# Performance work log

Hardware: AMD Instinct MI355X
Metric: run time of the kernel (lower is better)

Reference implementation:

```python
import jax, jax.numpy as jnp
import numpy as np

D_MODEL = 1024
D_STATE = 16
LN_EPS = 1e-5


def setup_inputs() -> dict:
    key = jax.random.key(0)
    ks = jax.random.split(key, 10)
    B, L, D, N = 4, 1024, D_MODEL, D_STATE
    s = lambda fan_in: 1.0 / np.sqrt(fan_in)
    x_in = jax.random.normal(ks[0], (B, L, D), dtype=jnp.float32)
    W_in = jax.random.uniform(ks[1], (D, 2 * D), jnp.float32, -s(D), s(D))
    W_x = jax.random.uniform(ks[2], (D, D + 2 * N), jnp.float32, -s(D), s(D))
    W_dt = jax.random.uniform(ks[3], (D, D), jnp.float32, -s(D), s(D))
    b_dt = jax.random.uniform(ks[4], (D,), jnp.float32, -4.0, -1.0)
    A_log = jnp.tile(jnp.log(jnp.arange(1, N + 1, dtype=jnp.float32))[None, :], (D, 1))
    D_param = jnp.ones((D,), dtype=jnp.float32)
    W_out = jax.random.uniform(ks[5], (D, D), jnp.float32, -s(D), s(D))
    ln_g = jnp.ones((D,), dtype=jnp.float32)
    ln_b = jnp.zeros((D,), dtype=jnp.float32)
    return {"x_in": x_in, "W_in": W_in, "W_x": W_x, "W_dt": W_dt, "b_dt": b_dt,
            "A_log": A_log, "D_param": D_param, "W_out": W_out, "ln_g": ln_g, "ln_b": ln_b}


def reference(x_in, W_in, W_x, W_dt, b_dt, A_log, D_param, W_out, ln_g, ln_b):
    B, L, D = x_in.shape
    N = A_log.shape[1]
    xz = x_in @ W_in                       # [B,L,2D]
    x, z = xz[..., :D], xz[..., D:]
    proj = x @ W_x                         # [B,L,D+2N]
    delta_raw = proj[..., :D]
    B_ssm = proj[..., D:D + N]
    C_ssm = proj[..., D + N:]
    delta = jax.nn.softplus(delta_raw @ W_dt + b_dt)   # [B,L,D]
    A = -jnp.exp(A_log)                    # [D,N]
    dA = jnp.exp(jnp.einsum('bld,dn->bldn', delta, A))      # [B,L,D,N]
    dBx = jnp.einsum('bld,bln->bldn', delta * x, B_ssm)      # dB * x, fused

    def step(h, inp):
        dA_t, dBx_t, C_t = inp             # [B,D,N],[B,D,N],[B,N]
        h = dA_t * h + dBx_t
        y_t = jnp.einsum('bdn,bn->bd', h, C_t)
        return h, y_t

    h0 = jnp.zeros((B, D, N), dtype=x.dtype)
    xs = (jnp.moveaxis(dA, 1, 0), jnp.moveaxis(dBx, 1, 0), jnp.moveaxis(C_ssm, 1, 0))
    _, ys = jax.lax.scan(step, h0, xs)     # ys: [L,B,D]
    y = jnp.moveaxis(ys, 0, 1) + x * D_param
    y = (y * jax.nn.silu(z)) @ W_out
    res = y + x_in
    mu = jnp.mean(res, axis=-1, keepdims=True)
    var = jnp.var(res, axis=-1, keepdims=True)
    return (res - mu) * jax.lax.rsqrt(var + LN_EPS) * ln_g + ln_b
```

## Files before the change

### kernel.cpp

```cpp
#include <hip/hip_runtime.h>

#define D_MODEL 1024
#define D_STATE 16
#define M_ROWS  4096
#define SEQ_L   1024
#define NSEG    32
#define LSEG    32

typedef __bf16 bf16x8 __attribute__((ext_vector_type(8)));
typedef float  f32x4  __attribute__((ext_vector_type(4)));

__device__ __forceinline__ unsigned short f2bf(float f) {
  unsigned int u = __builtin_bit_cast(unsigned int, f);
  u += 0x7fffu + ((u >> 16) & 1u);
  return (unsigned short)(u >> 16);
}
__device__ __forceinline__ float bf2f(unsigned short b) {
  unsigned int u = ((unsigned int)b) << 16;
  return __builtin_bit_cast(float, u);
}
__device__ __forceinline__ float load_elem(const void* p, size_t i, int isbf) {
  if (isbf) return bf2f(((const unsigned short*)p)[i]);
  return ((const float*)p)[i];
}

__device__ __forceinline__ void gload16(const void* g, void* l) {
  typedef const __attribute__((address_space(1))) unsigned int GU;
  typedef __attribute__((address_space(3))) unsigned int LU;
  __builtin_amdgcn_global_load_lds((GU*)(unsigned long long)g,
                                   (LU*)(unsigned int)(unsigned long long)l,
                                   16, 0, 0);
}

__global__ void detect_kernel(const unsigned short* __restrict__ x, int* __restrict__ flag) {
  __shared__ int cnt;
  if (threadIdx.x == 0) cnt = 0;
  __syncthreads();
  unsigned int v = x[2 * threadIdx.x];
  unsigned int e = (v >> 7) & 0xFFu;
  int ok = (e >= 100u && e <= 135u) ? 1 : 0;
  atomicAdd(&cnt, ok);
  __syncthreads();
  if (threadIdx.x == 0) *flag = (cnt >= 128) ? 1 : 0;
}

__global__ void convert_x_kernel(const void* __restrict__ src, float* __restrict__ dstf,
                                 unsigned short* __restrict__ dstb,
                                 const int* __restrict__ flag) {
  int c = blockIdx.x * blockDim.x + threadIdx.x;
  int isbf = *flag;
  float o[8];
  if (isbf) {
    uint4 v = ((const uint4*)src)[c];
    o[0] = bf2f((unsigned short)(v.x & 0xffffu)); o[1] = bf2f((unsigned short)(v.x >> 16));
    o[2] = bf2f((unsigned short)(v.y & 0xffffu)); o[3] = bf2f((unsigned short)(v.y >> 16));
    o[4] = bf2f((unsigned short)(v.z & 0xffffu)); o[5] = bf2f((unsigned short)(v.z >> 16));
    o[6] = bf2f((unsigned short)(v.w & 0xffffu)); o[7] = bf2f((unsigned short)(v.w >> 16));
    ((uint4*)dstb)[c] = v;
  } else {
    float4 a = ((const float4*)src)[2 * c];
    float4 b = ((const float4*)src)[2 * c + 1];
    o[0]=a.x; o[1]=a.y; o[2]=a.z; o[3]=a.w; o[4]=b.x; o[5]=b.y; o[6]=b.z; o[7]=b.w;
    uint4 p;
    p.x = (unsigned int)f2bf(o[0]) | ((unsigned int)f2bf(o[1]) << 16);
    p.y = (unsigned int)f2bf(o[2]) | ((unsigned int)f2bf(o[3]) << 16);
    p.z = (unsigned int)f2bf(o[4]) | ((unsigned int)f2bf(o[5]) << 16);
    p.w = (unsigned int)f2bf(o[6]) | ((unsigned int)f2bf(o[7]) << 16);
    ((uint4*)dstb)[c] = p;
  }
  float4* d = (float4*)dstf;
  d[2*c]   = make_float4(o[0], o[1], o[2], o[3]);
  d[2*c+1] = make_float4(o[4], o[5], o[6], o[7]);
}

__global__ void convert_smalls_kernel(const void* b_dt, const void* A_log, const void* Dp,
                                      const void* ln_g, const void* ln_b,
                                      float* o_bdt, float* o_a2, float* o_dp,
                                      float* o_lng, float* o_lnb,
                                      const int* __restrict__ flag) {
  int g = blockIdx.x * blockDim.x + threadIdx.x;
  int isbf = *flag;
  if (g < 1024)              o_bdt[g]          = load_elem(b_dt, g, isbf);
  else if (g < 17408) {
    float v = load_elem(A_log, g - 1024, isbf);
    o_a2[g - 1024] = -expf(v) * 1.4426950408889634f;
  }
  else if (g < 18432)        o_dp[g - 17408]   = load_elem(Dp, g - 17408, isbf);
  else if (g < 19456)        o_lng[g - 18432]  = load_elem(ln_g, g - 18432, isbf);
  else                       o_lnb[g - 19456]  = load_elem(ln_b, g - 19456, isbf);
}

__global__ void transpose_w_kernel(const void* __restrict__ src, unsigned short* __restrict__ dst,
                                   int ncols, const int* __restrict__ flag) {
  __shared__ float tile[32][33];
  int tx = threadIdx.x, ty = threadIdx.y;
  int n0 = blockIdx.x * 32, k0 = blockIdx.y * 32;
  int isbf = *flag;
  #pragma unroll
  for (int r = 0; r < 4; ++r) {
    int k = k0 + ty + r * 8;
    int n = n0 + tx;
    float v = (n < ncols) ? load_elem(src, (size_t)k * ncols + n, isbf) : 0.f;
    tile[ty + r * 8][tx] = v;
  }
  __syncthreads();
  #pragma unroll
  for (int r = 0; r < 4; ++r) {
    int n = n0 + ty + r * 8;
    int k = k0 + tx;
    dst[(size_t)n * 1024 + k] = f2bf(tile[tx][ty + r * 8]);
  }
}

template<int MODE>
__global__ __launch_bounds__(256, 3) void gemm_bf(
    const unsigned short* __restrict__ A, const unsigned short* __restrict__ Bt,
    void* __restrict__ o0, void* __restrict__ o1, float* __restrict__ o2f,
    const float* __restrict__ aux) {
  constexpr int NITER = D_MODEL / 32;
  __shared__ __align__(16) unsigned short a_lds[3][128 * 32];
  __shared__ __align__(16) unsigned short b_lds[3][128 * 32];
  const int tid = threadIdx.x;
  const int m0 = blockIdx.x * 128, n0 = blockIdx.y * 128;
  const int wave = tid >> 6, lane = tid & 63;
  const int wr = (wave >> 1) * 64, wc = (wave & 1) * 64;
  const int lrow = lane & 15, quad = lane >> 4;

  const int srow = wave * 32 + (lane >> 2);
  const int sc = (lane & 3) ^ ((lane >> 3) & 3);
  const unsigned short* gA  = A  + (size_t)(m0 + srow) * 1024 + sc * 8;
  const unsigned short* gA2 = gA + 16 * 1024;
  const unsigned short* gB  = Bt + (size_t)(n0 + srow) * 1024 + sc * 8;
  const unsigned short* gB2 = gB + 16 * 1024;
  const int soff = wave * 32 * 32;

  const int q2 = quad ^ ((lrow >> 1) & 3);

  f32x4 acc[4][4];
  #pragma unroll
  for (int i = 0; i < 4; ++i)
    #pragma unroll
    for (int jj = 0; jj < 4; ++jj)
      #pragma unroll
      for (int r = 0; r < 4; ++r) acc[i][jj][r] = 0.f;

  auto issue = [&](int k) {
    unsigned short* ab = &a_lds[k % 3][soff];
    unsigned short* bb = &b_lds[k % 3][soff];
    gload16(gA  + k * 32, ab);
    gload16(gA2 + k * 32, ab + 16 * 32);
    gload16(gB  + k * 32, bb);
    gload16(gB2 + k * 32, bb + 16 * 32);
  };
  auto compute = [&](int k) {
    const unsigned short* ard = &a_lds[k % 3][(wr + lrow) * 32 + q2 * 8];
    const unsigned short* brd = &b_lds[k % 3][(wc + lrow) * 32 + q2 * 8];
    bf16x8 af[4], bfr[4];
    #pragma unroll
    for (int i = 0; i < 4; ++i) {
      af[i]  = *(const bf16x8*)(ard + i * 16 * 32);
      bfr[i] = *(const bf16x8*)(brd + i * 16 * 32);
    }
    #pragma unroll
    for (int i = 0; i < 4; ++i)
      #pragma unroll
      for (int jj = 0; jj < 4; ++jj)
        acc[i][jj] = __builtin_amdgcn_mfma_f32_16x16x32_bf16(af[i], bfr[jj], acc[i][jj], 0, 0, 0);
  };

  issue(0);
  issue(1);
  #pragma unroll
  for (int k = 0; k < NITER - 1; ++k) {
    asm volatile("s_waitcnt vmcnt(4)" ::: "memory");
    __builtin_amdgcn_s_barrier();
    if (k + 2 < NITER) issue(k + 2);
    compute(k);
  }
  asm volatile("s_waitcnt vmcnt(0)" ::: "memory");
  __builtin_amdgcn_s_barrier();
  compute(NITER - 1);

  #pragma unroll
  for (int i = 0; i < 4; ++i) {
    #pragma unroll
    for (int jj = 0; jj < 4; ++jj) {
      #pragma unroll
      for (int r = 0; r < 4; ++r) {
        int m = m0 + wr + i * 16 + quad * 4 + r;
        int n = n0 + wc + jj * 16 + lrow;
        float v = acc[i][jj][r];
        if (MODE == 1) {
          if (n < D_MODEL) {
            ((unsigned short*)o0)[(size_t)m * D_MODEL + n] = f2bf(v);
          } else {
            float sig = 1.f / (1.f + expf(-v));
            ((unsigned short*)o1)[(size_t)m * D_MODEL + (n - D_MODEL)] = f2bf(v * sig);
          }
        } else if (MODE == 2) {
          if (n < D_MODEL)                  ((unsigned short*)o0)[(size_t)m * D_MODEL + n] = f2bf(v);
          else if (n < D_MODEL + D_STATE)   ((float*)o1)[(size_t)m * D_STATE + (n - D_MODEL)] = v;
          else if (n < D_MODEL + 2*D_STATE) o2f[(size_t)m * D_STATE + (n - D_MODEL - D_STATE)] = v;
        } else if (MODE == 3) {
          float t = v + aux[n];
          float sp = (t > 20.f) ? t : log1pf(expf(t));
          ((unsigned short*)o0)[(size_t)m * D_MODEL + n] = f2bf(sp);
        } else {
          ((float*)o0)[(size_t)m * D_MODEL + n] = v + aux[(size_t)m * D_MODEL + n];
        }
      }
    }
  }
}

template<int PHASE>
__global__ __launch_bounds__(256) void scan_phase(
    const unsigned short* __restrict__ dl_bf, const unsigned short* __restrict__ x_bf,
    const unsigned short* __restrict__ z_bf, const float* __restrict__ Bs,
    const float* __restrict__ Cs, const float* __restrict__ A2g,
    const float* __restrict__ Dpar, const float* __restrict__ hinit,
    float* __restrict__ Hout, float* __restrict__ sdout,
    unsigned short* __restrict__ g) {
  __shared__ float4 bsh[LSEG][4];
  __shared__ float4 csh[LSEG][4];
  const int tid = threadIdx.x;
  const int bid = blockIdx.x;
  const int seg = bid >> 4;
  const int b = (bid >> 2) & 3;
  const int dc = bid & 3;
  const int d = dc * 256 + tid;
  const int t0 = seg * LSEG;
  const int bd = b * D_MODEL + d;

  if (tid < 128) {
    int r = tid >> 2, q = tid & 3;
    size_t src = ((size_t)b * SEQ_L + t0 + r) * 4 + q;
    bsh[r][q] = ((const float4*)Bs)[src];
    if (PHASE == 1) csh[r][q] = ((const float4*)Cs)[src];
  }

  float A2r[16];
  {
    const float4* a4 = (const float4*)(A2g + (size_t)d * 16);
    #pragma unroll
    for (int q = 0; q < 4; ++q) {
      float4 v = a4[q];
      A2r[4*q] = v.x; A2r[4*q+1] = v.y; A2r[4*q+2] = v.z; A2r[4*q+3] = v.w;
    }
  }
  float h[16];
  if (PHASE == 1) {
    const float4* h4 = (const float4*)(hinit + (((size_t)seg * 4096) + bd) * 16);
    #pragma unroll
    for (int q = 0; q < 4; ++q) {
      float4 v = h4[q];
      h[4*q] = v.x; h[4*q+1] = v.y; h[4*q+2] = v.z; h[4*q+3] = v.w;
    }
  } else {
    #pragma unroll
    for (int n = 0; n < 16; ++n) h[n] = 0.f;
  }
  const float Dpd = (PHASE == 1) ? Dpar[d] : 0.f;
  float sd = 0.f;
  const size_t base = ((size_t)b * SEQ_L + t0) * D_MODEL + d;
  __syncthreads();

  unsigned short dreg[2][8], xreg[2][8], zreg[2][8];
  #pragma unroll
  for (int t = 0; t < 8; ++t) {
    size_t o = base + (size_t)t * D_MODEL;
    dreg[0][t] = dl_bf[o]; xreg[0][t] = x_bf[o];
    if (PHASE == 1) zreg[0][t] = z_bf[o];
  }
  #pragma unroll
  for (int c = 0; c < LSEG / 8; ++c) {
    const int cur = c & 1, nxt = cur ^ 1;
    if (c < LSEG / 8 - 1) {
      #pragma unroll
      for (int t = 0; t < 8; ++t) {
        size_t o = base + (size_t)((c + 1) * 8 + t) * D_MODEL;
        dreg[nxt][t] = dl_bf[o]; xreg[nxt][t] = x_bf[o];
        if (PHASE == 1) zreg[nxt][t] = z_bf[o];
      }
    }
    #pragma unroll
    for (int t = 0; t < 8; ++t) {
      const int tt = c * 8 + t;
      float dl = bf2f(dreg[cur][t]);
      float xx = bf2f(xreg[cur][t]);
      float dx = dl * xx;
      sd += dl;
      float4 b0 = bsh[tt][0], b1 = bsh[tt][1], b2 = bsh[tt][2], b3 = bsh[tt][3];
      float bb[16] = {b0.x,b0.y,b0.z,b0.w, b1.x,b1.y,b1.z,b1.w,
                      b2.x,b2.y,b2.z,b2.w, b3.x,b3.y,b3.z,b3.w};
      if (PHASE == 0) {
        #pragma unroll
        for (int n = 0; n < 16; ++n) {
          float dA = exp2f(dl * A2r[n]);
          h[n] = fmaf(dA, h[n], dx * bb[n]);
        }
      } else {
        float4 c0 = csh[tt][0], c1 = csh[tt][1], c2 = csh[tt][2], c3 = csh[tt][3];
        float cc[16] = {c0.x,c0.y,c0.z,c0.w, c1.x,c1.y,c1.z,c1.w,
                        c2.x,c2.y,c2.z,c2.w, c3.x,c3.y,c3.z,c3.w};
        float y = 0.f;
        #pragma unroll
        for (int n = 0; n < 16; ++n) {
          float dA = exp2f(dl * A2r[n]);
          h[n] = fmaf(dA, h[n], dx * bb[n]);
          y = fmaf(h[n], cc[n], y);
        }
        float zz = bf2f(zreg[cur][t]);
        g[base + (size_t)tt * D_MODEL] = f2bf(fmaf(xx, Dpd, y) * zz);
      }
    }
  }
  if (PHASE == 0) {
    float4* ho = (float4*)(Hout + (((size_t)seg * 4096) + bd) * 16);
    #pragma unroll
    for (int q = 0; q < 4; ++q)
      ho[q] = make_float4(h[4*q], h[4*q+1], h[4*q+2], h[4*q+3]);
    sdout[(size_t)seg * 4096 + bd] = sd;
  }
}

__global__ __launch_bounds__(256) void scan_phaseB(
    const float* __restrict__ H, const float* __restrict__ sdelta,
    const float* __restrict__ A2g, float* __restrict__ hinit) {
  int gidx = blockIdx.x * 256 + threadIdx.x;
  int bd = gidx >> 4, n = gidx & 15;
  float A2 = A2g[(size_t)(bd & (D_MODEL - 1)) * 16 + n];
  float hp = 0.f;
  #pragma unroll
  for (int s = 0; s < NSEG; ++s) {
    size_t idx = ((size_t)s * 4096 + bd) * 16 + n;
    hinit[idx] = hp;
    float P = exp2f(A2 * sdelta[(size_t)s * 4096 + bd]);
    hp = fmaf(P, hp, H[idx]);
  }
}

__global__ __launch_bounds__(256) void ln_kernel(const float* __restrict__ res,
    const float* __restrict__ lng, const float* __restrict__ lnb,
    void* __restrict__ out, const int* __restrict__ flag) {
  int row = blockIdx.x, tid = threadIdx.x;
  const float4* r4 = (const float4*)(res + (size_t)row * D_MODEL);
  float4 v = r4[tid];
  float s = v.x + v.y + v.z + v.w;
  float q = v.x * v.x + v.y * v.y + v.z * v.z + v.w * v.w;
  #pragma unroll
  for (int m = 1; m < 64; m <<= 1) { s += __shfl_xor(s, m); q += __shfl_xor(q, m); }
  __shared__ float ss[4], qs[4];
  int w = tid >> 6;
  if ((tid & 63) == 0) { ss[w] = s; qs[w] = q; }
  __syncthreads();
  s = ss[0] + ss[1] + ss[2] + ss[3];
  q = qs[0] + qs[1] + qs[2] + qs[3];
  float mu = s * (1.f / D_MODEL);
  float var = q * (1.f / D_MODEL) - mu * mu;
  float rstd = rsqrtf(var + 1e-5f);
  float4 gg = ((const float4*)lng)[tid];
  float4 bb = ((const float4*)lnb)[tid];
  float o0 = (v.x - mu) * rstd * gg.x + bb.x;
  float o1 = (v.y - mu) * rstd * gg.y + bb.y;
  float o2 = (v.z - mu) * rstd * gg.z + bb.z;
  float o3 = (v.w - mu) * rstd * gg.w + bb.w;
  if (*flag) {
    ushort4 pv;
    pv.x = f2bf(o0); pv.y = f2bf(o1); pv.z = f2bf(o2); pv.w = f2bf(o3);
    ((ushort4*)out)[(size_t)row * 256 + tid] = pv;
  } else {
    ((float4*)out)[(size_t)row * 256 + tid] = make_float4(o0, o1, o2, o3);
  }
}

extern "C" void kernel_launch(void* const* d_in, const int* in_sizes, int n_in,
                              void* d_out, int out_size, void* d_ws, size_t ws_size,
                              hipStream_t stream) {
  (void)in_sizes; (void)n_in; (void)out_size; (void)ws_size;
  const void* x_in  = d_in[0];
  const void* W_in  = d_in[1];
  const void* W_x   = d_in[2];
  const void* W_dt  = d_in[3];
  const void* b_dt  = d_in[4];
  const void* A_log = d_in[5];
  const void* D_par = d_in[6];
  const void* W_out = d_in[7];
  const void* ln_g  = d_in[8];
  const void* ln_b  = d_in[9];

  char* ws = (char*)d_ws;
  size_t off = 0;
  auto alloc = [&](size_t bytes) -> void* {
    void* p = ws + off;
    off += (bytes + 255) & ~(size_t)255;
    return p;
  };
  int* flag              = (int*)alloc(16);
  float* x_in_f          = (float*)alloc((size_t)M_ROWS * D_MODEL * 4);
  unsigned short* x_in_b = (unsigned short*)alloc((size_t)M_ROWS * D_MODEL * 2);
  float* bdt_f           = (float*)alloc(1024 * 4);
  float* a2_f            = (float*)alloc(16384 * 4);
  float* dp_f            = (float*)alloc(1024 * 4);
  float* lng_f           = (float*)alloc(1024 * 4);
  float* lnb_f           = (float*)alloc(1024 * 4);
  unsigned short* wt_in  = (unsigned short*)alloc((size_t)2048 * 1024 * 2);
  unsigned short* wt_x   = (unsigned short*)alloc((size_t)1152 * 1024 * 2);
  unsigned short* wt_dt  = (unsigned short*)alloc((size_t)1024 * 1024 * 2);
  unsigned short* wt_out = (unsigned short*)alloc((size_t)1024 * 1024 * 2);
  unsigned short* x_bf   = (unsigned short*)alloc((size_t)M_ROWS * D_MODEL * 2);
  unsigned short* s_bf   = (unsigned short*)alloc((size_t)M_ROWS * D_MODEL * 2);
  unsigned short* draw_bf= (unsigned short*)alloc((size_t)M_ROWS * D_MODEL * 2);
  unsigned short* delta_bf=(unsigned short*)alloc((size_t)M_ROWS * D_MODEL * 2);
  float* bssm_f          = (float*)alloc((size_t)M_ROWS * D_STATE * 4);
  float* cssm_f          = (float*)alloc((size_t)M_ROWS * D_STATE * 4);
  float* H_f             = (float*)alloc((size_t)NSEG * 4096 * 16 * 4);
  float* hinit_f         = (float*)alloc((size_t)NSEG * 4096 * 16 * 4);
  float* sdelta_f        = (float*)alloc((size_t)NSEG * 4096 * 4);
  unsigned short* g_bf = draw_bf;
  float* res_f = (float*)x_bf;

  detect_kernel<<<1, 256, 0, stream>>>((const unsigned short*)x_in, flag);
  convert_x_kernel<<<2048, 256, 0, stream>>>(x_in, x_in_f, x_in_b, flag);
  convert_smalls_kernel<<<80, 256, 0, stream>>>(b_dt, A_log, D_par, ln_g, ln_b,
                                                bdt_f, a2_f, dp_f, lng_f, lnb_f, flag);
  dim3 tb(32, 8);
  transpose_w_kernel<<<dim3(64, 32), tb, 0, stream>>>(W_in,  wt_in,  2048, flag);
  transpose_w_kernel<<<dim3(36, 32), tb, 0, stream>>>(W_x,   wt_x,   1056, flag);
  transpose_w_kernel<<<dim3(32, 32), tb, 0, stream>>>(W_dt,  wt_dt,  1024, flag);
  transpose_w_kernel<<<dim3(32, 32), tb, 0, stream>>>(W_out, wt_out, 1024, flag);

  gemm_bf<1><<<dim3(32, 16), 256, 0, stream>>>(x_in_b, wt_in, x_bf, s_bf, nullptr, nullptr);
  gemm_bf<2><<<dim3(32, 9),  256, 0, stream>>>(x_bf, wt_x, draw_bf, bssm_f, cssm_f, nullptr);
  gemm_bf<3><<<dim3(32, 8),  256, 0, stream>>>(draw_bf, wt_dt, delta_bf, nullptr, nullptr, bdt_f);

  scan_phase<0><<<512, 256, 0, stream>>>(delta_bf, x_bf, nullptr, bssm_f, nullptr,
                                         a2_f, nullptr, nullptr, H_f, sdelta_f, nullptr);
  scan_phaseB<<<256, 256, 0, stream>>>(H_f, sdelta_f, a2_f, hinit_f);
  scan_phase<1><<<512, 256, 0, stream>>>(delta_bf, x_bf, s_bf, bssm_f, cssm_f,
                                         a2_f, dp_f, hinit_f, nullptr, nullptr, g_bf);

  gemm_bf<4><<<dim3(32, 8),  256, 0, stream>>>(g_bf, wt_out, res_f, nullptr, nullptr, x_in_f);
  ln_kernel<<<4096, 256, 0, stream>>>(res_f, lng_f, lnb_f, d_out, flag);
}
```

Measured before the change: 289.1 us.

## Fold the input, x-projection and dt weights into one fused projection GEMM

Instead of chaining three activation GEMMs (x_in→xz, x→proj, delta_raw→delta), the product W_in·W_x·W_dt and the B/C column block of W_in·W_x are precomputed per call with small weight-only GEMMs. A single wide GEMM over x_in (N=3200) then produces x, silu(z), softplus delta, B and C in its epilogue. This removes activation-sized FLOPs, two launches and an intermediate buffer round-trip. In exchange it adds three low-occupancy weight GEMMs and extra bf16 rounding of the combined weights, which may change numerics.

```diff
diff --git a/kernel.cpp b/kernel.cpp
--- a/kernel.cpp
+++ b/kernel.cpp
@@ -73,6 +73,24 @@
   d[2*c+1] = make_float4(o[4], o[5], o[6], o[7]);
 }
 
+__global__ void convert_raw_kernel(const void* __restrict__ src, unsigned short* __restrict__ dst,
+                                   const int* __restrict__ flag) {
+  int c = blockIdx.x * blockDim.x + threadIdx.x;
+  int isbf = *flag;
+  if (isbf) {
+    ((uint4*)dst)[c] = ((const uint4*)src)[c];
+  } else {
+    float4 a = ((const float4*)src)[2 * c];
+    float4 b = ((const float4*)src)[2 * c + 1];
+    uint4 p;
+    p.x = (unsigned int)f2bf(a.x) | ((unsigned int)f2bf(a.y) << 16);
+    p.y = (unsigned int)f2bf(a.z) | ((unsigned int)f2bf(a.w) << 16);
+    p.z = (unsigned int)f2bf(b.x) | ((unsigned int)f2bf(b.y) << 16);
+    p.w = (unsigned int)f2bf(b.z) | ((unsigned int)f2bf(b.w) << 16);
+    ((uint4*)dst)[c] = p;
+  }
+}
+
 __global__ void convert_smalls_kernel(const void* b_dt, const void* A_log, const void* Dp,
                                       const void* ln_g, const void* ln_b,
                                       float* o_bdt, float* o_a2, float* o_dp,
@@ -91,10 +109,10 @@
 }
 
 __global__ void transpose_w_kernel(const void* __restrict__ src, unsigned short* __restrict__ dst,
-                                   int ncols, const int* __restrict__ flag) {
+                                   int ncols, int col0, const int* __restrict__ flag) {
   __shared__ float tile[32][33];
   int tx = threadIdx.x, ty = threadIdx.y;
-  int n0 = blockIdx.x * 32, k0 = blockIdx.y * 32;
+  int n0 = col0 + blockIdx.x * 32, k0 = blockIdx.y * 32;
   int isbf = *flag;
   #pragma unroll
   for (int r = 0; r < 4; ++r) {
@@ -108,14 +126,15 @@
   for (int r = 0; r < 4; ++r) {
     int n = n0 + ty + r * 8;
     int k = k0 + tx;
-    dst[(size_t)n * 1024 + k] = f2bf(tile[tx][ty + r * 8]);
+    dst[(size_t)(n - col0) * 1024 + k] = f2bf(tile[tx][ty + r * 8]);
   }
 }
 
 template<int MODE>
 __global__ __launch_bounds__(256, 3) void gemm_bf(
-    const unsigned short* __restrict__ A, const unsigned short* __restrict__ Bt,
-    void* __restrict__ o0, void* __restrict__ o1, float* __restrict__ o2f,
+    const unsigned short* __restrict__ A, const unsigned short* __restrict__ Bt, int ldb,
+    void* __restrict__ o0, void* __restrict__ o1, void* __restrict__ o2,
+    float* __restrict__ o3, float* __restrict__ o4,
     const float* __restrict__ aux) {
   constexpr int NITER = D_MODEL / 32;
   __shared__ __align__(16) unsigned short a_lds[3][128 * 32];
@@ -130,8 +149,8 @@
   const int sc = (lane & 3) ^ ((lane >> 3) & 3);
   const unsigned short* gA  = A  + (size_t)(m0 + srow) * 1024 + sc * 8;
   const unsigned short* gA2 = gA + 16 * 1024;
-  const unsigned short* gB  = Bt + (size_t)(n0 + srow) * 1024 + sc * 8;
-  const unsigned short* gB2 = gB + 16 * 1024;
+  const unsigned short* gB  = Bt + (size_t)(n0 + srow) * ldb + sc * 8;
+  const unsigned short* gB2 = gB + (size_t)16 * ldb;
   const int soff = wave * 32 * 32;
 
   const int q2 = quad ^ ((lrow >> 1) & 3);
@@ -190,23 +209,25 @@
         int m = m0 + wr + i * 16 + quad * 4 + r;
         int n = n0 + wc + jj * 16 + lrow;
         float v = acc[i][jj][r];
-        if (MODE == 1) {
-          if (n < D_MODEL) {
-            ((unsigned short*)o0)[(size_t)m * D_MODEL + n] = f2bf(v);
-          } else {
+        if (MODE == 0) {
+          ((unsigned short*)o0)[(size_t)m * 1024 + n] = f2bf(v);
+        } else if (MODE == 1) {
+          if (n < 1024) {
+            ((unsigned short*)o0)[(size_t)m * 1024 + n] = f2bf(v);
+          } else if (n < 2048) {
             float sig = 1.f / (1.f + expf(-v));
-            ((unsigned short*)o1)[(size_t)m * D_MODEL + (n - D_MODEL)] = f2bf(v * sig);
+            ((unsigned short*)o1)[(size_t)m * 1024 + (n - 1024)] = f2bf(v * sig);
+          } else if (n < 3072) {
+            float t = v + aux[n - 2048];
+            float sp = (t > 20.f) ? t : log1pf(expf(t));
+            ((unsigned short*)o2)[(size_t)m * 1024 + (n - 2048)] = f2bf(sp);
+          } else if (n < 3088) {
+            o3[(size_t)m * D_STATE + (n - 3072)] = v;
+          } else if (n < 3104) {
+            o4[(size_t)m * D_STATE + (n - 3088)] = v;
           }
-        } else if (MODE == 2) {
-          if (n < D_MODEL)                  ((unsigned short*)o0)[(size_t)m * D_MODEL + n] = f2bf(v);
-          else if (n < D_MODEL + D_STATE)   ((float*)o1)[(size_t)m * D_STATE + (n - D_MODEL)] = v;
-          else if (n < D_MODEL + 2*D_STATE) o2f[(size_t)m * D_STATE + (n - D_MODEL - D_STATE)] = v;
-        } else if (MODE == 3) {
-          float t = v + aux[n];
-          float sp = (t > 20.f) ? t : log1pf(expf(t));
-          ((unsigned short*)o0)[(size_t)m * D_MODEL + n] = f2bf(sp);
         } else {
-          ((float*)o0)[(size_t)m * D_MODEL + n] = v + aux[(size_t)m * D_MODEL + n];
+          ((float*)o0)[(size_t)m * 1024 + n] = v + aux[(size_t)m * 1024 + n];
         }
       }
     }
@@ -404,35 +425,45 @@
   float* dp_f            = (float*)alloc(1024 * 4);
   float* lng_f           = (float*)alloc(1024 * 4);
   float* lnb_f           = (float*)alloc(1024 * 4);
-  unsigned short* wt_in  = (unsigned short*)alloc((size_t)2048 * 1024 * 2);
-  unsigned short* wt_x   = (unsigned short*)alloc((size_t)1152 * 1024 * 2);
+  unsigned short* win_raw= (unsigned short*)alloc((size_t)1024 * 2048 * 2);
+  unsigned short* wx_raw = (unsigned short*)alloc((size_t)1024 * 1056 * 2);
   unsigned short* wt_dt  = (unsigned short*)alloc((size_t)1024 * 1024 * 2);
   unsigned short* wt_out = (unsigned short*)alloc((size_t)1024 * 1024 * 2);
+  unsigned short* wt_xbc = (unsigned short*)alloc((size_t)128 * 1024 * 2);
+  unsigned short* U_bf   = (unsigned short*)alloc((size_t)1024 * 1024 * 2);
+  unsigned short* btbig  = (unsigned short*)alloc((size_t)3200 * 1024 * 2);
   unsigned short* x_bf   = (unsigned short*)alloc((size_t)M_ROWS * D_MODEL * 2);
   unsigned short* s_bf   = (unsigned short*)alloc((size_t)M_ROWS * D_MODEL * 2);
-  unsigned short* draw_bf= (unsigned short*)alloc((size_t)M_ROWS * D_MODEL * 2);
   unsigned short* delta_bf=(unsigned short*)alloc((size_t)M_ROWS * D_MODEL * 2);
   float* bssm_f          = (float*)alloc((size_t)M_ROWS * D_STATE * 4);
   float* cssm_f          = (float*)alloc((size_t)M_ROWS * D_STATE * 4);
   float* H_f             = (float*)alloc((size_t)NSEG * 4096 * 16 * 4);
   float* hinit_f         = (float*)alloc((size_t)NSEG * 4096 * 16 * 4);
   float* sdelta_f        = (float*)alloc((size_t)NSEG * 4096 * 4);
-  unsigned short* g_bf = draw_bf;
+  unsigned short* g_bf   = (unsigned short*)alloc((size_t)M_ROWS * D_MODEL * 2);
   float* res_f = (float*)x_bf;
 
   detect_kernel<<<1, 256, 0, stream>>>((const unsigned short*)x_in, flag);
   convert_x_kernel<<<2048, 256, 0, stream>>>(x_in, x_in_f, x_in_b, flag);
   convert_smalls_kernel<<<80, 256, 0, stream>>>(b_dt, A_log, D_par, ln_g, ln_b,
                                                 bdt_f, a2_f, dp_f, lng_f, lnb_f, flag);
+  convert_raw_kernel<<<1024, 256, 0, stream>>>(W_in, win_raw, flag);
+  convert_raw_kernel<<<528, 256, 0, stream>>>(W_x, wx_raw, flag);
   dim3 tb(32, 8);
-  transpose_w_kernel<<<dim3(64, 32), tb, 0, stream>>>(W_in,  wt_in,  2048, flag);
-  transpose_w_kernel<<<dim3(36, 32), tb, 0, stream>>>(W_x,   wt_x,   1056, flag);
-  transpose_w_kernel<<<dim3(32, 32), tb, 0, stream>>>(W_dt,  wt_dt,  1024, flag);
-  transpose_w_kernel<<<dim3(32, 32), tb, 0, stream>>>(W_out, wt_out, 1024, flag);
-
-  gemm_bf<1><<<dim3(32, 16), 256, 0, stream>>>(x_in_b, wt_in, x_bf, s_bf, nullptr, nullptr);
-  gemm_bf<2><<<dim3(32, 9),  256, 0, stream>>>(x_bf, wt_x, draw_bf, bssm_f, cssm_f, nullptr);
-  gemm_bf<3><<<dim3(32, 8),  256, 0, stream>>>(draw_bf, wt_dt, delta_bf, nullptr, nullptr, bdt_f);
+  transpose_w_kernel<<<dim3(64, 32), tb, 0, stream>>>(W_in,  btbig,  2048, 0, flag);
+  transpose_w_kernel<<<dim3(4, 32),  tb, 0, stream>>>(W_x,   wt_xbc, 1056, 1024, flag);
+  transpose_w_kernel<<<dim3(32, 32), tb, 0, stream>>>(W_dt,  wt_dt,  1024, 0, flag);
+  transpose_w_kernel<<<dim3(32, 32), tb, 0, stream>>>(W_out, wt_out, 1024, 0, flag);
+
+  gemm_bf<0><<<dim3(8, 8), 256, 0, stream>>>(wt_dt, wx_raw, 1056, U_bf,
+                                             nullptr, nullptr, nullptr, nullptr, nullptr);
+  gemm_bf<0><<<dim3(8, 8), 256, 0, stream>>>(U_bf, win_raw, 2048, btbig + (size_t)2048 * 1024,
+                                             nullptr, nullptr, nullptr, nullptr, nullptr);
+  gemm_bf<0><<<dim3(1, 8), 256, 0, stream>>>(wt_xbc, win_raw, 2048, btbig + (size_t)3072 * 1024,
+                                             nullptr, nullptr, nullptr, nullptr, nullptr);
+
+  gemm_bf<1><<<dim3(32, 25), 256, 0, stream>>>(x_in_b, btbig, 1024,
+                                               x_bf, s_bf, delta_bf, bssm_f, cssm_f, bdt_f);
 
   scan_phase<0><<<512, 256, 0, stream>>>(delta_bf, x_bf, nullptr, bssm_f, nullptr,
                                          a2_f, nullptr, nullptr, H_f, sdelta_f, nullptr);
@@ -440,6 +471,7 @@
   scan_phase<1><<<512, 256, 0, stream>>>(delta_bf, x_bf, s_bf, bssm_f, cssm_f,
                                          a2_f, dp_f, hinit_f, nullptr, nullptr, g_bf);
 
-  gemm_bf<4><<<dim3(32, 8),  256, 0, stream>>>(g_bf, wt_out, res_f, nullptr, nullptr, x_in_f);
+  gemm_bf<4><<<dim3(32, 8), 256, 0, stream>>>(g_bf, wt_out, 1024,
+                                              res_f, nullptr, nullptr, nullptr, nullptr, x_in_f);
   ln_kernel<<<4096, 256, 0, stream>>>(res_f, lng_f, lnb_f, d_out, flag);
 }
```

Measured after the change: 303.2 us. 4.9% more time.
